# Kernel tuning notes

Hardware: AMD Instinct MI355X
Metric: run time of the kernel (lower is better)

## Reference

```python
import jax, jax.numpy as jnp
import numpy as np

N_EMBD = 2048
N_HEAD = 16
N_HIDDEN = 5632  # find_multiple(int(2*4*2048/3), 256)
EPS = 1e-5
BETA = 1.0


def rmsnorm(x, scale):
    # mean of squares computed in fp32 as in the torch code
    norm = jnp.mean(x.astype(jnp.float32) ** 2, axis=-1, keepdims=True)
    x_normed = x * jax.lax.rsqrt(norm + EPS)
    return (scale * x_normed).astype(x.dtype)


def setup_inputs() -> dict:
    key = jax.random.key(0)
    ks = jax.random.split(key, 9)
    B, T, C = 1, 2048, N_EMBD
    s = lambda k, shape, fan: jax.random.normal(k, shape, jnp.float32) * (1.0 / np.sqrt(fan))
    return {
        "x": jax.random.normal(ks[0], (B, T, C), jnp.float32),
        "alibi": jax.random.normal(ks[1], (N_HEAD, T, T), jnp.float32),
        "w_attn": s(ks[2], (C, 3 * C), C),   # c_attn weight (in, out) layout
        "w_proj": s(ks[3], (C, C), C),
        "w_fc1": s(ks[4], (C, N_HIDDEN), C),
        "w_fc2": s(ks[5], (C, N_HIDDEN), C),
        "w_mlp_proj": s(ks[6], (N_HIDDEN, C), N_HIDDEN),
        "rms1_scale": jnp.ones((C,), jnp.float32),
        "rms2_scale": jnp.ones((C,), jnp.float32),
    }


def attention(x, alibi, w_attn, w_proj):
    B, T, C = x.shape
    hd = C // N_HEAD
    qkv = x @ w_attn  # [B,T,3C]
    q, k, v = jnp.split(qkv, 3, axis=-1)
    q = q.reshape(B, T, N_HEAD, hd).transpose(0, 2, 1, 3)  # [B,H,T,hd]
    k = k.reshape(B, T, N_HEAD, hd).transpose(0, 2, 1, 3)
    v = v.reshape(B, T, N_HEAD, hd).transpose(0, 2, 1, 3)
    scale = 1.0 / np.sqrt(hd)
    scores = jnp.einsum("bhqd,bhkd->bhqk", q, k) * scale + BETA * alibi  # [B,H,T,T]
    causal = jnp.tril(jnp.ones((T, T), bool))
    scores = jnp.where(causal, scores, -jnp.inf)
    attn = jax.nn.softmax(scores, axis=-1)
    y = jnp.einsum("bhqk,bhkd->bhqd", attn, v)
    y = y.transpose(0, 2, 1, 3).reshape(B, T, C)
    return y @ w_proj


def mlp(x, w_fc1, w_fc2, w_mlp_proj):
    return (jax.nn.silu(x @ w_fc1) * (x @ w_fc2)) @ w_mlp_proj


def reference(x, alibi, w_attn, w_proj, w_fc1, w_fc2, w_mlp_proj, rms1_scale, rms2_scale):
    x = x + attention(rmsnorm(x, rms1_scale), alibi, w_attn, w_proj)
    x = x + mlp(rmsnorm(x, rms2_scale), w_fc1, w_fc2, w_mlp_proj)
    return x
```

## Files before the change

### kernel.cpp

```cpp
#include <hip/hip_runtime.h>
#include <stdint.h>

typedef __attribute__((ext_vector_type(4))) float f32x4;
typedef __attribute__((ext_vector_type(8))) __bf16 bf8_t;
typedef __attribute__((ext_vector_type(8))) uint16_t u16x8;

typedef __attribute__((address_space(1))) uint8_t as1_u8;
typedef __attribute__((address_space(3))) uint8_t as3_u8;

__device__ inline void async_copy16(const void* g, void* l) {
  __builtin_amdgcn_global_load_lds((const as1_u8*)g, (as3_u8*)l, 16, 0, 0);
}

__device__ inline uint16_t f2bf(float f) {
  uint32_t u = __builtin_bit_cast(uint32_t, f);
  u = (u + 0x7fff + ((u >> 16) & 1)) >> 16;
  return (uint16_t)u;
}
__device__ inline float bf2f(uint16_t h) {
  uint32_t u = ((uint32_t)h) << 16;
  return __builtin_bit_cast(float, u);
}
__device__ inline int swz(int r) { return (((r & 7) ^ ((r >> 3) & 7)) << 4); }
__device__ inline int vswz(int r) { return ((r & 7) << 4); }

__global__ __launch_bounds__(256) void rmsnorm_kernel(const float* __restrict__ X,
                                                      const float* __restrict__ S,
                                                      uint16_t* __restrict__ O) {
  const int row = blockIdx.x;
  const int tid = threadIdx.x;
  const float* xr = X + (size_t)row * 2048;
  float4 v1 = ((const float4*)xr)[tid * 2];
  float4 v2 = ((const float4*)xr)[tid * 2 + 1];
  float ss = v1.x * v1.x + v1.y * v1.y + v1.z * v1.z + v1.w * v1.w +
             v2.x * v2.x + v2.y * v2.y + v2.z * v2.z + v2.w * v2.w;
  #pragma unroll
  for (int m = 1; m < 64; m <<= 1) ss += __shfl_xor(ss, m);
  __shared__ float wsum[4];
  if ((tid & 63) == 0) wsum[tid >> 6] = ss;
  __syncthreads();
  float tot = wsum[0] + wsum[1] + wsum[2] + wsum[3];
  float inv = rsqrtf(tot * (1.0f / 2048.0f) + 1e-5f);
  const int base = tid * 8;
  const float* sc = S + base;
  float xs[8] = {v1.x, v1.y, v1.z, v1.w, v2.x, v2.y, v2.z, v2.w};
  u16x8 o;
  #pragma unroll
  for (int j = 0; j < 8; j++) o[j] = f2bf(xs[j] * inv * sc[j]);
  *(u16x8*)(O + (size_t)row * 2048 + base) = o;
}

__device__ inline void transpose_tile(const float* __restrict__ W, uint16_t* __restrict__ WT,
                                      int K, int N, int bx, int by, int tid) {
  __shared__ float tile[64][65];
  const int n0 = bx * 64, k0 = by * 64;
  const int lr = tid >> 4;
  const int lc = (tid & 15) * 4;
  #pragma unroll
  for (int i = 0; i < 4; i++) {
    const float4 v = *(const float4*)&W[(size_t)(k0 + lr + i * 16) * N + n0 + lc];
    tile[lr + i * 16][lc] = v.x;
    tile[lr + i * 16][lc + 1] = v.y;
    tile[lr + i * 16][lc + 2] = v.z;
    tile[lr + i * 16][lc + 3] = v.w;
  }
  __syncthreads();
  const int tn = tid >> 3;
  const int tk = (tid & 7) * 8;
  #pragma unroll
  for (int i = 0; i < 2; i++) {
    u16x8 o;
    #pragma unroll
    for (int j = 0; j < 8; j++) o[j] = f2bf(tile[tk + j][tn + i * 32]);
    *(u16x8*)&WT[(size_t)(n0 + tn + i * 32) * K + k0 + tk] = o;
  }
}

__global__ __launch_bounds__(256) void transpose_all(
    const float* __restrict__ w_attn, const float* __restrict__ w_proj,
    const float* __restrict__ w_fc1, const float* __restrict__ w_fc2,
    const float* __restrict__ w_mp,
    uint16_t* __restrict__ wt_attn, uint16_t* __restrict__ wt_proj,
    uint16_t* __restrict__ wt_fc1, uint16_t* __restrict__ wt_fc2,
    uint16_t* __restrict__ wt_mp) {
  int idx = blockIdx.x;
  const int tid = threadIdx.x;
  if (idx < 3072) {
    transpose_tile(w_attn, wt_attn, 2048, 6144, idx % 96, idx / 96, tid);
  } else if (idx < 4096) {
    idx -= 3072;
    transpose_tile(w_proj, wt_proj, 2048, 2048, idx % 32, idx / 32, tid);
  } else if (idx < 6912) {
    idx -= 4096;
    transpose_tile(w_fc1, wt_fc1, 2048, 5632, idx % 88, idx / 88, tid);
  } else if (idx < 9728) {
    idx -= 6912;
    transpose_tile(w_fc2, wt_fc2, 2048, 5632, idx % 88, idx / 88, tid);
  } else {
    idx -= 9728;
    transpose_tile(w_mp, wt_mp, 5632, 2048, idx % 32, idx / 32, tid);
  }
}

__global__ __launch_bounds__(256) void transpose_v(const uint16_t* __restrict__ qkv,
                                                   uint16_t* __restrict__ vT) {
  __shared__ uint16_t tile[64][68];
  const int t0 = blockIdx.x * 64;
  const int c0 = blockIdx.y * 64;
  const int tid = threadIdx.x;
  const int lr = tid >> 3;
  const int lc = (tid & 7) * 8;
  #pragma unroll
  for (int i = 0; i < 2; i++) {
    const int r = lr + i * 32;
    u16x8 v = *(const u16x8*)&qkv[(size_t)(t0 + r) * 6144 + 4096 + c0 + lc];
    #pragma unroll
    for (int j = 0; j < 8; j++) tile[lc + j][r] = v[j];
  }
  __syncthreads();
  #pragma unroll
  for (int i = 0; i < 2; i++) {
    const int c = lr + i * 32;
    u16x8 o = *(const u16x8*)&tile[c][lc];
    *(u16x8*)&vT[(size_t)(c0 + c) * 2048 + t0 + lc] = o;
  }
}

enum { EPI_BF16 = 0, EPI_ADDF32 = 1, EPI_SILUMUL = 2 };

__device__ inline void gemm_epi(int EPI, void* Cout, const void* RES, size_t idx, float v) {
  if (EPI == EPI_BF16) {
    ((uint16_t*)Cout)[idx] = f2bf(v);
  } else if (EPI == EPI_ADDF32) {
    ((float*)Cout)[idx] = ((const float*)RES)[idx] + v;
  } else {
    const float g = bf2f(((const uint16_t*)RES)[idx]);
    const float sg = g / (1.0f + __expf(-g));
    ((uint16_t*)Cout)[idx] = f2bf(sg * v);
  }
}

template <int EPI>
__global__ __launch_bounds__(256, 2) void gemm_bt(const uint16_t* __restrict__ A,
                                                  const uint16_t* __restrict__ BT,
                                                  void* __restrict__ Cout,
                                                  const void* __restrict__ RES,
                                                  int M, int N, int K) {
  __shared__ uint16_t As[128 * 32];
  __shared__ uint16_t Bs[128 * 32];
  const int tid = threadIdx.x;
  const int lane = tid & 63;
  const int w = tid >> 6;
  const int l15 = lane & 15, l4 = lane >> 4;
  const int m0 = blockIdx.y * 128, n0 = blockIdx.x * 128;
  const int wr = w >> 1, wc = w & 1;

  f32x4 acc[4][4];
  #pragma unroll
  for (int i = 0; i < 4; i++)
    #pragma unroll
    for (int j = 0; j < 4; j++) acc[i][j] = 0.0f;

  for (int kk = 0; kk < K; kk += 32) {
    __syncthreads();
    #pragma unroll
    for (int s = 0; s < 2; s++) {
      const int bu = s * 256 + w * 64;
      const int unit = bu + lane;
      const int row = unit >> 2, ch = unit & 3;
      async_copy16(A + (size_t)(m0 + row) * K + kk + ch * 8, (char*)As + bu * 16);
      async_copy16(BT + (size_t)(n0 + row) * K + kk + ch * 8, (char*)Bs + bu * 16);
    }
    __syncthreads();
    bf8_t a[4], b[4];
    #pragma unroll
    for (int mi = 0; mi < 4; mi++)
      a[mi] = *(const bf8_t*)(As + (wr * 64 + mi * 16 + l15) * 32 + l4 * 8);
    #pragma unroll
    for (int ni = 0; ni < 4; ni++)
      b[ni] = *(const bf8_t*)(Bs + (wc * 64 + ni * 16 + l15) * 32 + l4 * 8);
    #pragma unroll
    for (int mi = 0; mi < 4; mi++)
      #pragma unroll
      for (int ni = 0; ni < 4; ni++)
        acc[mi][ni] = __builtin_amdgcn_mfma_f32_16x16x32_bf16(a[mi], b[ni], acc[mi][ni], 0, 0, 0);
  }

  #pragma unroll
  for (int mi = 0; mi < 4; mi++) {
    #pragma unroll
    for (int ni = 0; ni < 4; ni++) {
      #pragma unroll
      for (int r = 0; r < 4; r++) {
        const int row = m0 + wr * 64 + mi * 16 + l4 * 4 + r;
        const int col = n0 + wc * 64 + ni * 16 + l15;
        gemm_epi(EPI, Cout, RES, (size_t)row * N + col, acc[mi][ni][r]);
      }
    }
  }
}

template <int EPI>
__global__ __launch_bounds__(256, 3) void gemm_bt64(const uint16_t* __restrict__ A,
                                                    const uint16_t* __restrict__ BT,
                                                    void* __restrict__ Cout,
                                                    const void* __restrict__ RES,
                                                    int M, int N, int K) {
  __shared__ uint16_t As[128 * 32];
  __shared__ uint16_t Bs[64 * 32];
  const int tid = threadIdx.x;
  const int lane = tid & 63;
  const int w = tid >> 6;
  const int l15 = lane & 15, l4 = lane >> 4;
  const int m0 = blockIdx.y * 128, n0 = blockIdx.x * 64;

  f32x4 acc[2][4];
  #pragma unroll
  for (int i = 0; i < 2; i++)
    #pragma unroll
    for (int j = 0; j < 4; j++) acc[i][j] = 0.0f;

  for (int kk = 0; kk < K; kk += 32) {
    __syncthreads();
    #pragma unroll
    for (int s = 0; s < 2; s++) {
      const int bu = s * 256 + w * 64;
      const int unit = bu + lane;
      const int row = unit >> 2, ch = unit & 3;
      async_copy16(A + (size_t)(m0 + row) * K + kk + ch * 8, (char*)As + bu * 16);
    }
    {
      const int bu = w * 64;
      const int unit = bu + lane;
      const int row = unit >> 2, ch = unit & 3;
      async_copy16(BT + (size_t)(n0 + row) * K + kk + ch * 8, (char*)Bs + bu * 16);
    }
    __syncthreads();
    bf8_t a[2], b[4];
    #pragma unroll
    for (int mi = 0; mi < 2; mi++)
      a[mi] = *(const bf8_t*)(As + (w * 32 + mi * 16 + l15) * 32 + l4 * 8);
    #pragma unroll
    for (int ni = 0; ni < 4; ni++)
      b[ni] = *(const bf8_t*)(Bs + (ni * 16 + l15) * 32 + l4 * 8);
    #pragma unroll
    for (int mi = 0; mi < 2; mi++)
      #pragma unroll
      for (int ni = 0; ni < 4; ni++)
        acc[mi][ni] = __builtin_amdgcn_mfma_f32_16x16x32_bf16(a[mi], b[ni], acc[mi][ni], 0, 0, 0);
  }

  #pragma unroll
  for (int mi = 0; mi < 2; mi++) {
    #pragma unroll
    for (int ni = 0; ni < 4; ni++) {
      #pragma unroll
      for (int r = 0; r < 4; r++) {
        const int row = m0 + w * 32 + mi * 16 + l4 * 4 + r;
        const int col = n0 + ni * 16 + l15;
        gemm_epi(EPI, Cout, RES, (size_t)row * N + col, acc[mi][ni][r]);
      }
    }
  }
}

#define PART_STRIDE (64 * 128 + 128)
__global__ __launch_bounds__(256, 2) void attn_part(const uint16_t* __restrict__ qkv,
                                                    const uint16_t* __restrict__ vT,
                                                    const float* __restrict__ alibi,
                                                    float* __restrict__ part) {
  const int p = blockIdx.x;
  const int qt = 31 - blockIdx.y;
  const int h = blockIdx.z;
  const int c = (qt + 4) >> 2;
  const int start = p * c;
  const int end = min((p + 1) * c, qt + 1);
  if (start >= end) return;

  const int tid = threadIdx.x;
  const int lane = tid & 63;
  const int w = tid >> 6;
  const int l15 = lane & 15, l4 = lane >> 4;

  __shared__ uint16_t Ks[2][64 * 128];
  __shared__ uint16_t Vs[2][128 * 64];
  __shared__ uint16_t Ps[4][16 * 64];

  const float scale = 0.08838834764831845f;

  auto stage = [&](int kv0, int b) {
    #pragma unroll
    for (int i = 0; i < 4; i++) {
      const int u = tid + i * 256;
      const int r = u >> 4;
      const int cc = (u & 15) ^ ((r & 7) ^ ((r >> 3) & 7));
      async_copy16(qkv + (size_t)(kv0 + r) * 6144 + 2048 + h * 128 + cc * 8,
                   (char*)Ks[b] + u * 16);
    }
    #pragma unroll
    for (int i = 0; i < 4; i++) {
      const int u = tid + i * 256;
      const int r = u >> 3;
      const int cc = (u & 7) ^ (r & 7);
      async_copy16(vT + (size_t)(h * 128 + r) * 2048 + kv0 + cc * 8,
                   (char*)Vs[b] + u * 16);
    }
  };
  auto load_al = [&](int kv0, float (&al)[4][4]) {
    #pragma unroll
    for (int r = 0; r < 4; r++) {
      const size_t rowb = ((size_t)h * 2048 + (qt * 64 + w * 16 + l4 * 4 + r)) * 2048;
      #pragma unroll
      for (int nf = 0; nf < 4; nf++)
        al[nf][r] = alibi[rowb + kv0 + nf * 16 + l15];
    }
  };

  const int qrow = qt * 64 + w * 16 + l15;
  bf8_t qf[4];
  #pragma unroll
  for (int kc = 0; kc < 4; kc++)
    qf[kc] = *(const bf8_t*)(qkv + (size_t)qrow * 6144 + h * 128 + kc * 32 + l4 * 8);

  f32x4 accy[8];
  #pragma unroll
  for (int i = 0; i < 8; i++) accy[i] = 0.0f;
  float mrun[4], lrun[4];
  #pragma unroll
  for (int r = 0; r < 4; r++) { mrun[r] = -1e30f; lrun[r] = 0.0f; }

  stage(start * 64, 0);
  float al[4][4];
  load_al(start * 64, al);

  for (int kvt = start; kvt < end; kvt++) {
    const int b = (kvt - start) & 1;
    const int kv0 = kvt * 64;
    __syncthreads();

    const int kvn = (kvt + 1 < end) ? (kvt + 1) : kvt;
    float aln[4][4];
    load_al(kvn * 64, aln);
    stage(kvn * 64, b ^ 1);

    float s[4][4];
    #pragma unroll
    for (int nf = 0; nf < 4; nf++) {
      f32x4 sa = 0.0f;
      const int krow = nf * 16 + l15;
      __builtin_amdgcn_s_setprio(1);
      #pragma unroll
      for (int kc = 0; kc < 4; kc++) {
        bf8_t kb = *(const bf8_t*)((const char*)Ks[b] +
                                   ((krow * 256 + kc * 64 + l4 * 16) ^ swz(krow)));
        sa = __builtin_amdgcn_mfma_f32_16x16x32_bf16(qf[kc], kb, sa, 0, 0, 0);
      }
      __builtin_amdgcn_s_setprio(0);
      const int kvcol = kv0 + nf * 16 + l15;
      #pragma unroll
      for (int r = 0; r < 4; r++) {
        const int q = qt * 64 + w * 16 + l4 * 4 + r;
        float sv = sa[r] * scale + al[nf][r];
        if (kvcol > q) sv = -1e30f;
        s[nf][r] = sv;
      }
    }

    #pragma unroll
    for (int r = 0; r < 4; r++) {
      float rm = fmaxf(fmaxf(s[0][r], s[1][r]), fmaxf(s[2][r], s[3][r]));
      rm = fmaxf(rm, __shfl_xor(rm, 1));
      rm = fmaxf(rm, __shfl_xor(rm, 2));
      rm = fmaxf(rm, __shfl_xor(rm, 4));
      rm = fmaxf(rm, __shfl_xor(rm, 8));
      const float mnew = fmaxf(mrun[r], rm);
      const float alpha = __expf(mrun[r] - mnew);
      mrun[r] = mnew;
      float rs = 0.0f;
      #pragma unroll
      for (int nf = 0; nf < 4; nf++) {
        const float pp = __expf(s[nf][r] - mnew);
        s[nf][r] = pp;
        rs += pp;
      }
      rs += __shfl_xor(rs, 1);
      rs += __shfl_xor(rs, 2);
      rs += __shfl_xor(rs, 4);
      rs += __shfl_xor(rs, 8);
      lrun[r] = lrun[r] * alpha + rs;
      #pragma unroll
      for (int df = 0; df < 8; df++) accy[df][r] *= alpha;
    }

    #pragma unroll
    for (int nf = 0; nf < 4; nf++) {
      #pragma unroll
      for (int r = 0; r < 4; r++) {
        const int rq = l4 * 4 + r;
        const int bo = (rq * 128 + (nf * 16 + l15) * 2) ^ vswz(rq);
        *(uint16_t*)((char*)Ps[w] + bo) = f2bf(s[nf][r]);
      }
    }

    __builtin_amdgcn_s_setprio(1);
    #pragma unroll
    for (int kk = 0; kk < 2; kk++) {
      bf8_t pa = *(const bf8_t*)((const char*)Ps[w] +
                                 ((l15 * 128 + kk * 64 + l4 * 16) ^ vswz(l15)));
      #pragma unroll
      for (int df = 0; df < 8; df++) {
        const int vr = df * 16 + l15;
        bf8_t vb = *(const bf8_t*)((const char*)Vs[b] +
                                   ((vr * 128 + kk * 64 + l4 * 16) ^ vswz(vr)));
        accy[df] = __builtin_amdgcn_mfma_f32_16x16x32_bf16(pa, vb, accy[df], 0, 0, 0);
      }
    }
    __builtin_amdgcn_s_setprio(0);

    #pragma unroll
    for (int nf = 0; nf < 4; nf++)
      #pragma unroll
      for (int r = 0; r < 4; r++) al[nf][r] = aln[nf][r];
  }

  float* pb = part + (size_t)(((h * 32 + qt) * 4) + p) * PART_STRIDE;
  #pragma unroll
  for (int df = 0; df < 8; df++) {
    #pragma unroll
    for (int r = 0; r < 4; r++) {
      const int row = w * 16 + l4 * 4 + r;
      pb[row * 128 + df * 16 + l15] = accy[df][r];
    }
  }
  if (l15 == 0) {
    #pragma unroll
    for (int r = 0; r < 4; r++) {
      const int row = w * 16 + l4 * 4 + r;
      pb[8192 + row] = mrun[r];
      pb[8192 + 64 + row] = lrun[r];
    }
  }
}

__global__ __launch_bounds__(256) void attn_merge(const float* __restrict__ part,
                                                  uint16_t* __restrict__ Y) {
  const int qt = blockIdx.x;
  const int h = blockIdx.y;
  const int c = (qt + 4) >> 2;
  const int cnt = (qt + c) / c;
  const int tid = threadIdx.x;
  const int row = tid >> 2;
  const int cg = (tid & 3) * 32;

  const float* pb = part + (size_t)((h * 32 + qt) * 4) * PART_STRIDE;

  float m_p[4], w_p[4];
  float M = -1e30f;
  for (int p = 0; p < cnt; p++) {
    m_p[p] = pb[p * PART_STRIDE + 8192 + row];
    M = fmaxf(M, m_p[p]);
  }
  float L = 0.0f;
  for (int p = 0; p < cnt; p++) {
    w_p[p] = __expf(m_p[p] - M);
    L += w_p[p] * pb[p * PART_STRIDE + 8192 + 64 + row];
  }
  const float invL = 1.0f / L;

  uint16_t* yr = Y + (size_t)(qt * 64 + row) * 2048 + h * 128 + cg;
  #pragma unroll
  for (int j = 0; j < 32; j += 8) {
    f32x4 s0 = 0.0f, s1 = 0.0f;
    for (int p = 0; p < cnt; p++) {
      const float* ap = pb + p * PART_STRIDE + row * 128 + cg + j;
      s0 += w_p[p] * *(const f32x4*)ap;
      s1 += w_p[p] * *(const f32x4*)(ap + 4);
    }
    u16x8 o;
    #pragma unroll
    for (int e = 0; e < 4; e++) { o[e] = f2bf(s0[e] * invL); o[e + 4] = f2bf(s1[e] * invL); }
    *(u16x8*)(yr + j) = o;
  }
}

extern "C" void kernel_launch(void* const* d_in, const int* in_sizes, int n_in,
                              void* d_out, int out_size, void* d_ws, size_t ws_size,
                              hipStream_t stream) {
  const float* x      = (const float*)d_in[0];
  const float* alibi  = (const float*)d_in[1];
  const float* w_attn = (const float*)d_in[2];
  const float* w_proj = (const float*)d_in[3];
  const float* w_fc1  = (const float*)d_in[4];
  const float* w_fc2  = (const float*)d_in[5];
  const float* w_mp   = (const float*)d_in[6];
  const float* rms1   = (const float*)d_in[7];
  const float* rms2   = (const float*)d_in[8];
  float* out = (float*)d_out;

  char* ws = (char*)d_ws;
  uint16_t* xn      = (uint16_t*)(ws + 0);
  uint16_t* qkv     = (uint16_t*)(ws + 8388608);
  uint16_t* y       = (uint16_t*)(ws + 33554432);
  uint16_t* g1      = (uint16_t*)(ws + 41943040);
  uint16_t* hbuf    = (uint16_t*)(ws + 65011712);
  uint16_t* wt_attn = (uint16_t*)(ws + 88080384);
  uint16_t* wt_proj = (uint16_t*)(ws + 113246208);
  uint16_t* wt_fc1  = (uint16_t*)(ws + 121634816);
  uint16_t* wt_fc2  = (uint16_t*)(ws + 144703488);
  uint16_t* wt_mp   = (uint16_t*)(ws + 167772160);
  uint16_t* vT      = (uint16_t*)(ws + 190840832);
  float*    part    = (float*)(ws + 199229440);

  transpose_all<<<12544, 256, 0, stream>>>(w_attn, w_proj, w_fc1, w_fc2, w_mp,
                                           wt_attn, wt_proj, wt_fc1, wt_fc2, wt_mp);

  rmsnorm_kernel<<<2048, 256, 0, stream>>>(x, rms1, xn);

  gemm_bt<EPI_BF16><<<dim3(6144 / 128, 2048 / 128), 256, 0, stream>>>(
      xn, wt_attn, qkv, nullptr, 2048, 6144, 2048);

  transpose_v<<<dim3(32, 32), 256, 0, stream>>>(qkv, vT);

  attn_part<<<dim3(4, 32, 16), 256, 0, stream>>>(qkv, vT, alibi, part);

  attn_merge<<<dim3(32, 16), 256, 0, stream>>>(part, y);

  gemm_bt64<EPI_ADDF32><<<dim3(2048 / 64, 2048 / 128), 256, 0, stream>>>(
      y, wt_proj, out, x, 2048, 2048, 2048);

  rmsnorm_kernel<<<2048, 256, 0, stream>>>(out, rms2, xn);

  gemm_bt<EPI_BF16><<<dim3(5632 / 128, 2048 / 128), 256, 0, stream>>>(
      xn, wt_fc1, g1, nullptr, 2048, 5632, 2048);

  gemm_bt<EPI_SILUMUL><<<dim3(5632 / 128, 2048 / 128), 256, 0, stream>>>(
      xn, wt_fc2, hbuf, g1, 2048, 5632, 2048);

  gemm_bt64<EPI_ADDF32><<<dim3(2048 / 64, 2048 / 128), 256, 0, stream>>>(
      hbuf, wt_mp, out, out, 2048, 2048, 5632);
}
```

Before: 562.5 us.

## Fuse fc1/fc2 GEMMs with SiLU and compute V transposed directly

Replaces the two MLP up-projection GEMMs plus SiLU-multiply epilogue with one kernel that accumulates both products against a shared A tile and applies SiLU*mul in registers. This removes the g1 round-trip through memory and the second read of the activations. The QKV GEMM now produces only Q and K, and V^T is computed directly as W_v^T · xn^T, which drops the separate transpose_v kernel. The fused MLP kernel holds two 4x4 accumulator sets, which raises register pressure and may lower occupancy. It also loads A and both B tiles without double buffering.

```diff
diff --git a/kernel.cpp b/kernel.cpp
--- a/kernel.cpp
+++ b/kernel.cpp
@@ -102,30 +102,6 @@
   }
 }
 
-__global__ __launch_bounds__(256) void transpose_v(const uint16_t* __restrict__ qkv,
-                                                   uint16_t* __restrict__ vT) {
-  __shared__ uint16_t tile[64][68];
-  const int t0 = blockIdx.x * 64;
-  const int c0 = blockIdx.y * 64;
-  const int tid = threadIdx.x;
-  const int lr = tid >> 3;
-  const int lc = (tid & 7) * 8;
-  #pragma unroll
-  for (int i = 0; i < 2; i++) {
-    const int r = lr + i * 32;
-    u16x8 v = *(const u16x8*)&qkv[(size_t)(t0 + r) * 6144 + 4096 + c0 + lc];
-    #pragma unroll
-    for (int j = 0; j < 8; j++) tile[lc + j][r] = v[j];
-  }
-  __syncthreads();
-  #pragma unroll
-  for (int i = 0; i < 2; i++) {
-    const int c = lr + i * 32;
-    u16x8 o = *(const u16x8*)&tile[c][lc];
-    *(u16x8*)&vT[(size_t)(c0 + c) * 2048 + t0 + lc] = o;
-  }
-}
-
 enum { EPI_BF16 = 0, EPI_ADDF32 = 1, EPI_SILUMUL = 2 };
 
 __device__ inline void gemm_epi(int EPI, void* Cout, const void* RES, size_t idx, float v) {
@@ -264,8 +240,75 @@
   }
 }
 
+__global__ __launch_bounds__(256, 2) void gemm_mlp(const uint16_t* __restrict__ A,
+                                                   const uint16_t* __restrict__ B1T,
+                                                   const uint16_t* __restrict__ B2T,
+                                                   uint16_t* __restrict__ Cout,
+                                                   int M, int N, int K) {
+  __shared__ uint16_t As[128 * 32];
+  __shared__ uint16_t B1s[128 * 32];
+  __shared__ uint16_t B2s[128 * 32];
+  const int tid = threadIdx.x;
+  const int lane = tid & 63;
+  const int w = tid >> 6;
+  const int l15 = lane & 15, l4 = lane >> 4;
+  const int m0 = blockIdx.y * 128, n0 = blockIdx.x * 128;
+  const int wr = w >> 1, wc = w & 1;
+
+  f32x4 acc1[4][4], acc2[4][4];
+  #pragma unroll
+  for (int i = 0; i < 4; i++)
+    #pragma unroll
+    for (int j = 0; j < 4; j++) { acc1[i][j] = 0.0f; acc2[i][j] = 0.0f; }
+
+  for (int kk = 0; kk < K; kk += 32) {
+    __syncthreads();
+    #pragma unroll
+    for (int s = 0; s < 2; s++) {
+      const int bu = s * 256 + w * 64;
+      const int unit = bu + lane;
+      const int row = unit >> 2, ch = unit & 3;
+      async_copy16(A + (size_t)(m0 + row) * K + kk + ch * 8, (char*)As + bu * 16);
+      async_copy16(B1T + (size_t)(n0 + row) * K + kk + ch * 8, (char*)B1s + bu * 16);
+      async_copy16(B2T + (size_t)(n0 + row) * K + kk + ch * 8, (char*)B2s + bu * 16);
+    }
+    __syncthreads();
+    bf8_t a[4], b1[4], b2[4];
+    #pragma unroll
+    for (int mi = 0; mi < 4; mi++)
+      a[mi] = *(const bf8_t*)(As + (wr * 64 + mi * 16 + l15) * 32 + l4 * 8);
+    #pragma unroll
+    for (int ni = 0; ni < 4; ni++) {
+      b1[ni] = *(const bf8_t*)(B1s + (wc * 64 + ni * 16 + l15) * 32 + l4 * 8);
+      b2[ni] = *(const bf8_t*)(B2s + (wc * 64 + ni * 16 + l15) * 32 + l4 * 8);
+    }
+    #pragma unroll
+    for (int mi = 0; mi < 4; mi++)
+      #pragma unroll
+      for (int ni = 0; ni < 4; ni++) {
+        acc1[mi][ni] = __builtin_amdgcn_mfma_f32_16x16x32_bf16(a[mi], b1[ni], acc1[mi][ni], 0, 0, 0);
+        acc2[mi][ni] = __builtin_amdgcn_mfma_f32_16x16x32_bf16(a[mi], b2[ni], acc2[mi][ni], 0, 0, 0);
+      }
+  }
+
+  #pragma unroll
+  for (int mi = 0; mi < 4; mi++) {
+    #pragma unroll
+    for (int ni = 0; ni < 4; ni++) {
+      #pragma unroll
+      for (int r = 0; r < 4; r++) {
+        const int row = m0 + wr * 64 + mi * 16 + l4 * 4 + r;
+        const int col = n0 + wc * 64 + ni * 16 + l15;
+        const float g = acc1[mi][ni][r];
+        const float sg = g / (1.0f + __expf(-g));
+        Cout[(size_t)row * N + col] = f2bf(sg * acc2[mi][ni][r]);
+      }
+    }
+  }
+}
+
 #define PART_STRIDE (64 * 128 + 128)
-__global__ __launch_bounds__(256, 2) void attn_part(const uint16_t* __restrict__ qkv,
+__global__ __launch_bounds__(256, 2) void attn_part(const uint16_t* __restrict__ qk,
                                                     const uint16_t* __restrict__ vT,
                                                     const float* __restrict__ alibi,
                                                     float* __restrict__ part) {
@@ -294,7 +337,7 @@
       const int u = tid + i * 256;
       const int r = u >> 4;
       const int cc = (u & 15) ^ ((r & 7) ^ ((r >> 3) & 7));
-      async_copy16(qkv + (size_t)(kv0 + r) * 6144 + 2048 + h * 128 + cc * 8,
+      async_copy16(qk + (size_t)(kv0 + r) * 4096 + 2048 + h * 128 + cc * 8,
                    (char*)Ks[b] + u * 16);
     }
     #pragma unroll
@@ -320,7 +363,7 @@
   bf8_t qf[4];
   #pragma unroll
   for (int kc = 0; kc < 4; kc++)
-    qf[kc] = *(const bf8_t*)(qkv + (size_t)qrow * 6144 + h * 128 + kc * 32 + l4 * 8);
+    qf[kc] = *(const bf8_t*)(qk + (size_t)qrow * 4096 + h * 128 + kc * 32 + l4 * 8);
 
   f32x4 accy[8];
   #pragma unroll
@@ -499,9 +542,8 @@
 
   char* ws = (char*)d_ws;
   uint16_t* xn      = (uint16_t*)(ws + 0);
-  uint16_t* qkv     = (uint16_t*)(ws + 8388608);
+  uint16_t* qk      = (uint16_t*)(ws + 8388608);
   uint16_t* y       = (uint16_t*)(ws + 33554432);
-  uint16_t* g1      = (uint16_t*)(ws + 41943040);
   uint16_t* hbuf    = (uint16_t*)(ws + 65011712);
   uint16_t* wt_attn = (uint16_t*)(ws + 88080384);
   uint16_t* wt_proj = (uint16_t*)(ws + 113246208);
@@ -516,12 +558,13 @@
 
   rmsnorm_kernel<<<2048, 256, 0, stream>>>(x, rms1, xn);
 
-  gemm_bt<EPI_BF16><<<dim3(6144 / 128, 2048 / 128), 256, 0, stream>>>(
-      xn, wt_attn, qkv, nullptr, 2048, 6144, 2048);
-
-  transpose_v<<<dim3(32, 32), 256, 0, stream>>>(qkv, vT);
-
-  attn_part<<<dim3(4, 32, 16), 256, 0, stream>>>(qkv, vT, alibi, part);
+  gemm_bt<EPI_BF16><<<dim3(4096 / 128, 2048 / 128), 256, 0, stream>>>(
+      xn, wt_attn, qk, nullptr, 2048, 4096, 2048);
+
+  gemm_bt64<EPI_BF16><<<dim3(2048 / 64, 2048 / 128), 256, 0, stream>>>(
+      wt_attn + (size_t)4096 * 2048, xn, vT, nullptr, 2048, 2048, 2048);
+
+  attn_part<<<dim3(4, 32, 16), 256, 0, stream>>>(qk, vT, alibi, part);
 
   attn_merge<<<dim3(32, 16), 256, 0, stream>>>(part, y);
 
@@ -530,11 +573,8 @@
 
   rmsnorm_kernel<<<2048, 256, 0, stream>>>(out, rms2, xn);
 
-  gemm_bt<EPI_BF16><<<dim3(5632 / 128, 2048 / 128), 256, 0, stream>>>(
-      xn, wt_fc1, g1, nullptr, 2048, 5632, 2048);
-
-  gemm_bt<EPI_SILUMUL><<<dim3(5632 / 128, 2048 / 128), 256, 0, stream>>>(
-      xn, wt_fc2, hbuf, g1, 2048, 5632, 2048);
+  gemm_mlp<<<dim3(5632 / 128, 2048 / 128), 256, 0, stream>>>(
+      xn, wt_fc1, wt_fc2, hbuf, 2048, 5632, 2048);
 
   gemm_bt64<EPI_ADDF32><<<dim3(2048 / 64, 2048 / 128), 256, 0, stream>>>(
       hbuf, wt_mp, out, out, 2048, 2048, 5632);
```

New measurement: 603.4 us. 1.07x slower.
